# Kernel tuning notes

Measured on AMD Instinct MI355X. Metric: run time of the kernel, lower is better.

## Reference

```python
import jax, jax.numpy as jnp
import numpy as np

DIM = 512
NUM_HEADS = 16
HEAD_DIM = DIM // NUM_HEADS
HIDDEN = int(DIM * 4.0)
EPS = 1e-5


def layer_norm(x, gamma, beta):
    mu = jnp.mean(x, axis=-1, keepdims=True)
    var = jnp.mean(jnp.square(x - mu), axis=-1, keepdims=True)
    return (x - mu) * jax.lax.rsqrt(var + EPS) * gamma + beta


def setup_inputs() -> dict:
    key = jax.random.key(0)
    ks = jax.random.split(key, 8)
    B, L, C = 32, 3136, DIM
    x = jax.random.normal(ks[0], (B, L, C), dtype=jnp.float32)
    norm1_g = jnp.ones((C,), jnp.float32)
    norm1_b = jnp.zeros((C,), jnp.float32)
    # spatial (per-head) mixing weight: (num_heads, head_dim, head_dim)
    w_spatial = jax.random.normal(ks[1], (NUM_HEADS, HEAD_DIM, HEAD_DIM), jnp.float32) * (1.0 / np.sqrt(HEAD_DIM))
    norm2_g = jnp.ones((C,), jnp.float32)
    norm2_b = jnp.zeros((C,), jnp.float32)
    w1 = jax.random.normal(ks[2], (C, HIDDEN), jnp.float32) * (1.0 / np.sqrt(C))
    b1 = jnp.zeros((HIDDEN,), jnp.float32)
    w2 = jax.random.normal(ks[3], (HIDDEN, C), jnp.float32) * (1.0 / np.sqrt(HIDDEN))
    b2 = jnp.zeros((C,), jnp.float32)
    return {"x": x, "norm1_g": norm1_g, "norm1_b": norm1_b, "w_spatial": w_spatial,
            "norm2_g": norm2_g, "norm2_b": norm2_b, "w1": w1, "b1": b1, "w2": w2, "b2": b2}


def reference(x, norm1_g, norm1_b, w_spatial, norm2_g, norm2_b, w1, b1, w2, b2):
    B, L, C = x.shape
    shortcut = x
    h = layer_norm(x, norm1_g, norm1_b)
    # window partition -> per-head channel-sub-dim linear (shared across windows/positions)
    # mathematically equivalent to applying the per-head matmul at every token
    h = h.reshape(B, L, NUM_HEADS, HEAD_DIM)
    h = jnp.einsum('blhd,hde->blhe', h, w_spatial)
    h = h.reshape(B, L, C)
    x = shortcut + h
    # channel MLP: Linear -> GELU(tanh) -> Linear
    y = layer_norm(x, norm2_g, norm2_b)
    y = jax.nn.gelu(y @ w1 + b1, approximate=True)
    y = y @ w2 + b2
    return x + y
```

## Files before the change

### kernel.cpp

```cpp
#include <hip/hip_runtime.h>
#include <hip/hip_bf16.h>


typedef __bf16 bf16x8 __attribute__((ext_vector_type(8)));
typedef float f32x4 __attribute__((ext_vector_type(4)));

constexpr int CDIM = 512;
constexpr int HID = 2048;
constexpr int MROWS = 32 * 3136;
constexpr float LN_EPS = 1e-5f;

static __device__ __forceinline__ float gelu_tanh(float x) {
  const float u = 0.7978845608028654f * fmaf(0.044715f * x * x, x, x);
  const float e = __expf(2.0f * u);
  return 0.5f * x * (2.0f - 2.0f / (e + 1.0f));
}

static __device__ __forceinline__ void load_lds16(const void* g, void* l) {
  __builtin_amdgcn_global_load_lds((__attribute__((address_space(1))) void*)g,
                                   (__attribute__((address_space(3))) void*)l,
                                   16, 0, 0);
}

template <int KD>
__global__ __launch_bounds__(256) void cvt_t(const float* __restrict__ src,
                                             __hip_bfloat16* __restrict__ dst,
                                             int ND) {
  const int i = blockIdx.x * 256 + threadIdx.x;
  const int n = i / KD;
  const int k = i - n * KD;
  dst[i] = __float2bfloat16(src[(size_t)k * ND + n]);
}

__global__ __launch_bounds__(256) void fused_pre(
    const float* __restrict__ x, const float* __restrict__ g1,
    const float* __restrict__ b1, const float* __restrict__ wsp,
    const float* __restrict__ g2, const float* __restrict__ b2,
    float* __restrict__ x2out, __hip_bfloat16* __restrict__ yout) {
  __shared__ float lnbuf[CDIM];
  __shared__ float red[8];

  const int t = threadIdx.x;
  const int lane = t & 63;
  const int w = t >> 6;
  const int c0 = t, c1 = t + 256;
  const int hd0 = c0 >> 5, e0 = c0 & 31;
  const int hd1 = c1 >> 5, e1 = c1 & 31;

  float wc0[32], wc1[32];
#pragma unroll
  for (int d = 0; d < 32; ++d) {
    wc0[d] = wsp[(hd0 * 32 + d) * 32 + e0];
    wc1[d] = wsp[(hd1 * 32 + d) * 32 + e1];
  }
  const float g1v0 = g1[c0], g1v1 = g1[c1], b1v0 = b1[c0], b1v1 = b1[c1];
  const float g2v0 = g2[c0], g2v1 = g2[c1], b2v0 = b2[c0], b2v1 = b2[c1];

  for (int r = blockIdx.x; r < MROWS; r += gridDim.x) {
    const float* xr = x + (size_t)r * CDIM;
    const float xv0 = xr[c0], xv1 = xr[c1];

    float s = xv0 + xv1, ss = xv0 * xv0 + xv1 * xv1;
#pragma unroll
    for (int off = 32; off; off >>= 1) {
      s += __shfl_down(s, off);
      ss += __shfl_down(ss, off);
    }
    if (lane == 0) { red[w * 2] = s; red[w * 2 + 1] = ss; }
    __syncthreads();
    s = red[0] + red[2] + red[4] + red[6];
    ss = red[1] + red[3] + red[5] + red[7];
    float mu = s * (1.0f / CDIM);
    float var = ss * (1.0f / CDIM) - mu * mu;
    float rs = rsqrtf(var + LN_EPS);
    lnbuf[c0] = (xv0 - mu) * rs * g1v0 + b1v0;
    lnbuf[c1] = (xv1 - mu) * rs * g1v1 + b1v1;
    __syncthreads();

    float h0 = 0.f, h1 = 0.f;
#pragma unroll
    for (int d = 0; d < 32; ++d) {
      h0 = fmaf(lnbuf[hd0 * 32 + d], wc0[d], h0);
      h1 = fmaf(lnbuf[hd1 * 32 + d], wc1[d], h1);
    }
    const float a0 = xv0 + h0, a1 = xv1 + h1;
    x2out[(size_t)r * CDIM + c0] = a0;
    x2out[(size_t)r * CDIM + c1] = a1;

    s = a0 + a1;
    ss = a0 * a0 + a1 * a1;
#pragma unroll
    for (int off = 32; off; off >>= 1) {
      s += __shfl_down(s, off);
      ss += __shfl_down(ss, off);
    }
    if (lane == 0) { red[w * 2] = s; red[w * 2 + 1] = ss; }
    __syncthreads();
    s = red[0] + red[2] + red[4] + red[6];
    ss = red[1] + red[3] + red[5] + red[7];
    mu = s * (1.0f / CDIM);
    var = ss * (1.0f / CDIM) - mu * mu;
    rs = rsqrtf(var + LN_EPS);
    yout[(size_t)r * CDIM + c0] = __float2bfloat16((a0 - mu) * rs * g2v0 + b2v0);
    yout[(size_t)r * CDIM + c1] = __float2bfloat16((a1 - mu) * rs * g2v1 + b2v1);
    __syncthreads();
  }
}

template <int K, int N, bool GELU>
__global__ __launch_bounds__(256) void gemm_bt(
    const __hip_bfloat16* __restrict__ A, const __hip_bfloat16* __restrict__ Bt,
    const float* __restrict__ bias, __hip_bfloat16* __restrict__ zout,
    float* __restrict__ fout) {
  constexpr int NT = N / 128;
  __shared__ __attribute__((aligned(16))) __hip_bfloat16 As[128 * 32];
  __shared__ __attribute__((aligned(16))) __hip_bfloat16 Bs[128 * 32];

  const int tid = threadIdx.x;
  const int lane = tid & 63;
  const int w = tid >> 6;
  const int wr = w >> 1, wc = w & 1;

  const int cpx = gridDim.x >> 3;
  const int bid = (blockIdx.x & 7) * cpx + (blockIdx.x >> 3);

  const int tm = bid / NT;
  const int tn = bid - tm * NT;
  const size_t am0 = (size_t)tm * 128;
  const int bn0 = tn * 128;

  const int s0 = w * 64 + lane;
  const int r0 = s0 >> 2, k0 = (s0 & 3) * 8;
  const int s1 = s0 + 256;
  const int r1 = s1 >> 2, k1 = (s1 & 3) * 8;
  const __hip_bfloat16* a0p = A + (am0 + r0) * K + k0;
  const __hip_bfloat16* a1p = A + (am0 + r1) * K + k1;
  const __hip_bfloat16* b0p = Bt + (size_t)(bn0 + r0) * K + k0;
  const __hip_bfloat16* b1p = Bt + (size_t)(bn0 + r1) * K + k1;
  __hip_bfloat16* lA0 = As + (size_t)(w * 64) * 8;
  __hip_bfloat16* lA1 = As + (size_t)(w * 64 + 256) * 8;
  __hip_bfloat16* lB0 = Bs + (size_t)(w * 64) * 8;
  __hip_bfloat16* lB1 = Bs + (size_t)(w * 64 + 256) * 8;

  f32x4 acc[4][4] = {};
  const int fr = lane & 15;
  const int kg = (lane >> 4) * 8;

  for (int kt = 0; kt < K / 32; ++kt) {
    const int kb = kt * 32;
    load_lds16(a0p + kb, lA0);
    load_lds16(a1p + kb, lA1);
    load_lds16(b0p + kb, lB0);
    load_lds16(b1p + kb, lB1);
    __syncthreads();

    bf16x8 af[4], bfv[4];
#pragma unroll
    for (int m = 0; m < 4; ++m)
      af[m] = *(const bf16x8*)(As + (wr * 64 + m * 16 + fr) * 32 + kg);
#pragma unroll
    for (int n = 0; n < 4; ++n)
      bfv[n] = *(const bf16x8*)(Bs + (wc * 64 + n * 16 + fr) * 32 + kg);
#pragma unroll
    for (int m = 0; m < 4; ++m)
#pragma unroll
      for (int n = 0; n < 4; ++n)
        acc[m][n] = __builtin_amdgcn_mfma_f32_16x16x32_bf16(af[m], bfv[n],
                                                            acc[m][n], 0, 0, 0);
    __syncthreads();
  }

  const int cr = (lane >> 4) * 4;
  const int cc = lane & 15;
#pragma unroll
  for (int n = 0; n < 4; ++n) {
    const int col = bn0 + wc * 64 + n * 16 + cc;
    const float bv = bias[col];
#pragma unroll
    for (int m = 0; m < 4; ++m) {
      const size_t row = am0 + wr * 64 + m * 16 + cr;
#pragma unroll
      for (int j = 0; j < 4; ++j) {
        const float v = acc[m][n][j] + bv;
        const size_t off = (row + j) * N + col;
        if constexpr (GELU) {
          zout[off] = __float2bfloat16(gelu_tanh(v));
        } else {
          fout[off] = fout[off] + v;
        }
      }
    }
  }
}

extern "C" void kernel_launch(void* const* d_in, const int* in_sizes, int n_in,
                              void* d_out, int out_size, void* d_ws,
                              size_t ws_size, hipStream_t stream) {
  const float* x = (const float*)d_in[0];
  const float* n1g = (const float*)d_in[1];
  const float* n1b = (const float*)d_in[2];
  const float* wsp = (const float*)d_in[3];
  const float* n2g = (const float*)d_in[4];
  const float* n2b = (const float*)d_in[5];
  const float* w1 = (const float*)d_in[6];
  const float* b1 = (const float*)d_in[7];
  const float* w2 = (const float*)d_in[8];
  const float* b2 = (const float*)d_in[9];
  float* out = (float*)d_out;

  __hip_bfloat16* ybuf = (__hip_bfloat16*)d_ws;
  __hip_bfloat16* zbuf = ybuf + (size_t)MROWS * CDIM;
  __hip_bfloat16* w1t = zbuf + (size_t)MROWS * HID;
  __hip_bfloat16* w2t = w1t + (size_t)CDIM * HID;

  cvt_t<CDIM><<<(CDIM * HID) / 256, 256, 0, stream>>>(w1, w1t, HID);
  cvt_t<HID><<<(CDIM * HID) / 256, 256, 0, stream>>>(w2, w2t, CDIM);
  fused_pre<<<2048, 256, 0, stream>>>(x, n1g, n1b, wsp, n2g, n2b, out, ybuf);
  gemm_bt<CDIM, HID, true><<<(MROWS / 128) * (HID / 128), 256, 0, stream>>>(
      ybuf, w1t, b1, zbuf, nullptr);
  gemm_bt<HID, CDIM, false><<<(MROWS / 128) * (CDIM / 128), 256, 0, stream>>>(
      zbuf, w2t, b2, nullptr, out);
}
```

Measured before the change: 1.030 ms.

## Rewrite GEMMs as 256x256 8-wave tiles with 4-slot LDS pipelining and swizzle

Replaces the 128x128, 4-wave GEMM with a 256x256 tile computed by 8 waves. The tile is fed by a 4-slot LDS ring that prefetches two K-steps ahead using direct global-to-LDS loads and explicit vmcnt waits. K-chunks are XOR-swizzled in LDS to avoid bank conflicts, and MFMA sections are wrapped in s_setprio. The aim is to hide global load latency, increase data reuse per tile and cut barrier stalls, at the cost of larger register and LDS use per block (128 KB LDS) and fewer blocks per CU.

New measurement: 939.3 us. 8.8% less time.

```diff
diff --git a/kernel.cpp b/kernel.cpp
--- a/kernel.cpp
+++ b/kernel.cpp
@@ -108,77 +108,111 @@
 }
 
 template <int K, int N, bool GELU>
-__global__ __launch_bounds__(256) void gemm_bt(
+__global__ __launch_bounds__(512, 2) void gemm8p(
     const __hip_bfloat16* __restrict__ A, const __hip_bfloat16* __restrict__ Bt,
     const float* __restrict__ bias, __hip_bfloat16* __restrict__ zout,
     float* __restrict__ fout) {
-  constexpr int NT = N / 128;
-  __shared__ __attribute__((aligned(16))) __hip_bfloat16 As[128 * 32];
-  __shared__ __attribute__((aligned(16))) __hip_bfloat16 Bs[128 * 32];
+  constexpr int NT = N / 256;
+  constexpr int NKT = K / 32;
+  __shared__ __attribute__((aligned(16))) __hip_bfloat16 lds[4][2][256 * 32];
 
   const int tid = threadIdx.x;
   const int lane = tid & 63;
   const int w = tid >> 6;
-  const int wr = w >> 1, wc = w & 1;
+  const int wm = w >> 2, wn = w & 3;
 
   const int cpx = gridDim.x >> 3;
   const int bid = (blockIdx.x & 7) * cpx + (blockIdx.x >> 3);
-
-  const int tm = bid / NT;
-  const int tn = bid - tm * NT;
-  const size_t am0 = (size_t)tm * 128;
-  const int bn0 = tn * 128;
-
-  const int s0 = w * 64 + lane;
-  const int r0 = s0 >> 2, k0 = (s0 & 3) * 8;
-  const int s1 = s0 + 256;
-  const int r1 = s1 >> 2, k1 = (s1 & 3) * 8;
-  const __hip_bfloat16* a0p = A + (am0 + r0) * K + k0;
-  const __hip_bfloat16* a1p = A + (am0 + r1) * K + k1;
-  const __hip_bfloat16* b0p = Bt + (size_t)(bn0 + r0) * K + k0;
-  const __hip_bfloat16* b1p = Bt + (size_t)(bn0 + r1) * K + k1;
-  __hip_bfloat16* lA0 = As + (size_t)(w * 64) * 8;
-  __hip_bfloat16* lA1 = As + (size_t)(w * 64 + 256) * 8;
-  __hip_bfloat16* lB0 = Bs + (size_t)(w * 64) * 8;
-  __hip_bfloat16* lB1 = Bs + (size_t)(w * 64 + 256) * 8;
-
-  f32x4 acc[4][4] = {};
+  const int tm = bid / NT, tn = bid - tm * NT;
+  const size_t am0 = (size_t)tm * 256;
+  const int bn0 = tn * 256;
+
+  const int r0 = tid >> 2;
+  const int ks0 = (tid & 3) ^ ((tid >> 2) & 3) ^ ((tid >> 4) & 3);
+  const __hip_bfloat16* aP0 = A + (am0 + r0) * K + ks0 * 8;
+  const __hip_bfloat16* aP1 = aP0 + (size_t)128 * K;
+  const __hip_bfloat16* bP0 = Bt + (size_t)(bn0 + r0) * K + ks0 * 8;
+  const __hip_bfloat16* bP1 = bP0 + (size_t)128 * K;
+  const int lo0 = (w * 64) * 8;
+  const int lo1 = (512 + w * 64) * 8;
+
+#define STAGE_A(sl, kt)                            \
+  do {                                             \
+    load_lds16(aP0 + (kt) * 32, &lds[sl][0][lo0]); \
+    load_lds16(aP1 + (kt) * 32, &lds[sl][0][lo1]); \
+  } while (0)
+#define STAGE_B(sl, kt)                            \
+  do {                                             \
+    load_lds16(bP0 + (kt) * 32, &lds[sl][1][lo0]); \
+    load_lds16(bP1 + (kt) * 32, &lds[sl][1][lo1]); \
+  } while (0)
+
+  f32x4 acc[8][4] = {};
   const int fr = lane & 15;
-  const int kg = (lane >> 4) * 8;
-
-  for (int kt = 0; kt < K / 32; ++kt) {
-    const int kb = kt * 32;
-    load_lds16(a0p + kb, lA0);
-    load_lds16(a1p + kb, lA1);
-    load_lds16(b0p + kb, lB0);
-    load_lds16(b1p + kb, lB1);
-    __syncthreads();
-
-    bf16x8 af[4], bfv[4];
-#pragma unroll
-    for (int m = 0; m < 4; ++m)
-      af[m] = *(const bf16x8*)(As + (wr * 64 + m * 16 + fr) * 32 + kg);
+  const int kgs = (((lane >> 4) ^ (lane & 3) ^ ((lane >> 2) & 3))) * 8;
+
+  STAGE_A(0, 0);
+  STAGE_B(0, 0);
+  STAGE_A(1, 1);
+  STAGE_B(1, 1);
+
+  for (int t = 0; t < NKT; ++t) {
+    if (t + 1 < NKT)
+      asm volatile("s_waitcnt vmcnt(4)" ::: "memory");
+    else
+      asm volatile("s_waitcnt vmcnt(0)" ::: "memory");
+    __builtin_amdgcn_s_barrier();
+
+    const int sl = t & 3;
+    const int s2 = (t + 2) & 3;
+    const bool pf = (t + 2) < NKT;
+    const __hip_bfloat16* As = lds[sl][0];
+    const __hip_bfloat16* Bs = lds[sl][1];
+
+    if (pf) STAGE_A(s2, t + 2);
+    bf16x8 bfv[4];
 #pragma unroll
     for (int n = 0; n < 4; ++n)
-      bfv[n] = *(const bf16x8*)(Bs + (wc * 64 + n * 16 + fr) * 32 + kg);
+      bfv[n] = *(const bf16x8*)(Bs + (wn * 64 + n * 16 + fr) * 32 + kgs);
+    bf16x8 af[4];
+#pragma unroll
+    for (int m = 0; m < 4; ++m)
+      af[m] = *(const bf16x8*)(As + (wm * 128 + m * 16 + fr) * 32 + kgs);
+    __builtin_amdgcn_s_setprio(1);
 #pragma unroll
     for (int m = 0; m < 4; ++m)
 #pragma unroll
       for (int n = 0; n < 4; ++n)
         acc[m][n] = __builtin_amdgcn_mfma_f32_16x16x32_bf16(af[m], bfv[n],
                                                             acc[m][n], 0, 0, 0);
-    __syncthreads();
-  }
+    __builtin_amdgcn_s_setprio(0);
+    __builtin_amdgcn_s_barrier();
+
+    if (pf) STAGE_B(s2, t + 2);
+#pragma unroll
+    for (int m = 0; m < 4; ++m)
+      af[m] = *(const bf16x8*)(As + (wm * 128 + (m + 4) * 16 + fr) * 32 + kgs);
+    __builtin_amdgcn_s_setprio(1);
+#pragma unroll
+    for (int m = 0; m < 4; ++m)
+#pragma unroll
+      for (int n = 0; n < 4; ++n)
+        acc[m + 4][n] = __builtin_amdgcn_mfma_f32_16x16x32_bf16(
+            af[m], bfv[n], acc[m + 4][n], 0, 0, 0);
+    __builtin_amdgcn_s_setprio(0);
+  }
+#undef STAGE_A
+#undef STAGE_B
 
   const int cr = (lane >> 4) * 4;
   const int cc = lane & 15;
 #pragma unroll
   for (int n = 0; n < 4; ++n) {
-    const int col = bn0 + wc * 64 + n * 16 + cc;
+    const int col = bn0 + wn * 64 + n * 16 + cc;
     const float bv = bias[col];
 #pragma unroll
-    for (int m = 0; m < 4; ++m) {
-      const size_t row = am0 + wr * 64 + m * 16 + cr;
+    for (int m = 0; m < 8; ++m) {
+      const size_t row = am0 + wm * 128 + m * 16 + cr;
 #pragma unroll
       for (int j = 0; j < 4; ++j) {
         const float v = acc[m][n][j] + bv;
@@ -216,8 +250,8 @@
   cvt_t<CDIM><<<(CDIM * HID) / 256, 256, 0, stream>>>(w1, w1t, HID);
   cvt_t<HID><<<(CDIM * HID) / 256, 256, 0, stream>>>(w2, w2t, CDIM);
   fused_pre<<<2048, 256, 0, stream>>>(x, n1g, n1b, wsp, n2g, n2b, out, ybuf);
-  gemm_bt<CDIM, HID, true><<<(MROWS / 128) * (HID / 128), 256, 0, stream>>>(
+  gemm8p<CDIM, HID, true><<<(MROWS / 256) * (HID / 256), 512, 0, stream>>>(
       ybuf, w1t, b1, zbuf, nullptr);
-  gemm_bt<HID, CDIM, false><<<(MROWS / 128) * (CDIM / 128), 256, 0, stream>>>(
+  gemm8p<HID, CDIM, false><<<(MROWS / 256) * (CDIM / 256), 512, 0, stream>>>(
       zbuf, w2t, b2, nullptr, out);
 }
```
